# Performance work log

Hardware: AMD Instinct MI355X
Metric: run time of the kernel (lower is better)

The kernel has to match this reference:

```python
import jax, jax.numpy as jnp
import numpy as np

N, E = 50000, 800000
IN_D, HID, H1, OUT_D, H2, EDGE_D = 64, 16, 8, 64, 2, 1
NEG_SLOPE = 0.2


def gatv2_layer(x, src, dst, edge_attr, Wl, Wr, We, att, bias, concat):
    """PyG GATv2Conv (add_self_loops=False, share_weights=False), eval mode (no dropout)."""
    n = x.shape[0]
    H, C = att.shape
    xl = (x @ Wl).reshape(n, H, C)            # source transform
    xr = (x @ Wr).reshape(n, H, C)            # target transform
    ee = (edge_attr @ We).reshape(-1, H, C)   # edge embedding
    z = jax.nn.leaky_relu(xl[src] + xr[dst] + ee, NEG_SLOPE)  # [E,H,C]
    score = jnp.einsum('ehc,hc->eh', z, att)                  # [E,H]
    # softmax over incoming edges per target node
    m = jax.ops.segment_max(score, dst, num_segments=n)
    m = jnp.where(jnp.isfinite(m), m, 0.0)
    a = jnp.exp(score - m[dst])
    denom = jax.ops.segment_sum(a, dst, num_segments=n)
    alpha = a / (denom[dst] + 1e-16)                          # [E,H]
    msg = xl[src] * alpha[..., None]                          # [E,H,C]
    out = jax.ops.segment_sum(msg, dst, num_segments=n)       # [N,H,C]
    if concat:
        return out.reshape(n, H * C) + bias
    return out.mean(axis=1) + bias


def layer_norm(x, g, b):
    mu = x.mean(-1, keepdims=True)
    var = ((x - mu) ** 2).mean(-1, keepdims=True)
    return (x - mu) * jax.lax.rsqrt(var + 1e-5) * g + b


def setup_inputs() -> dict:
    key = jax.random.key(0)
    ks = jax.random.split(key, 24)
    def w(k, *shape):
        fan_in = shape[0]
        return jax.random.normal(k, shape, dtype=jnp.float32) * (1.0 / np.sqrt(fan_in))
    inp = {
        'x': jax.random.normal(ks[0], (N, IN_D), dtype=jnp.float32),
        'edge_index': jax.random.randint(ks[1], (2, E), 0, N, dtype=jnp.int64),
        'edge_attr': jax.random.normal(ks[2], (E, EDGE_D), dtype=jnp.float32),
        # layer 1 (heads=8, out=16, concat)
        'w1_l': w(ks[3], IN_D, H1 * HID), 'w1_r': w(ks[4], IN_D, H1 * HID),
        'w1_e': w(ks[5], EDGE_D, H1 * HID),
        'att1': jax.random.normal(ks[6], (H1, HID), dtype=jnp.float32) * 0.1,
        'b1': jnp.zeros((H1 * HID,), dtype=jnp.float32),
        # layer 2 (heads=2, out=64, mean)
        'w2_l': w(ks[7], H1 * HID, H2 * OUT_D), 'w2_r': w(ks[8], H1 * HID, H2 * OUT_D),
        'w2_e': w(ks[9], EDGE_D, H2 * OUT_D),
        'att2': jax.random.normal(ks[10], (H2, OUT_D), dtype=jnp.float32) * 0.1,
        'b2': jnp.zeros((OUT_D,), dtype=jnp.float32),
        # classifier: Linear + LayerNorm + GELU + ResidualBlockv2
        'wc': w(ks[11], OUT_D, OUT_D), 'bc': jnp.zeros((OUT_D,), dtype=jnp.float32),
        'ln_g': jnp.ones((OUT_D,), dtype=jnp.float32), 'ln_b': jnp.zeros((OUT_D,), dtype=jnp.float32),
        'wr': w(ks[12], OUT_D, OUT_D), 'br': jnp.zeros((OUT_D,), dtype=jnp.float32),
        'lnr_g': jnp.ones((OUT_D,), dtype=jnp.float32), 'lnr_b': jnp.zeros((OUT_D,), dtype=jnp.float32),
    }
    return inp


def reference(x, edge_index, edge_attr, w1_l, w1_r, w1_e, att1, b1,
              w2_l, w2_r, w2_e, att2, b2, wc, bc, ln_g, ln_b, wr, br, lnr_g, lnr_b):
    src, dst = edge_index[0], edge_index[1]
    h = jax.nn.relu(gatv2_layer(x, src, dst, edge_attr, w1_l, w1_r, w1_e, att1, b1, True))
    h = jax.nn.relu(gatv2_layer(h, src, dst, edge_attr, w2_l, w2_r, w2_e, att2, b2, False))
    h = jax.nn.gelu(layer_norm(h @ wc + bc, ln_g, ln_b), approximate=False)
    # ResidualBlockv2: Linear -> LayerNorm -> GELU with residual skip
    h = h + jax.nn.gelu(layer_norm(h @ wr + br, lnr_g, lnr_b), approximate=False)
    return h
```

## Files before the change

### kernel.cpp

```cpp
#include <hip/hip_runtime.h>
#include <math.h>

#define NNODE 50000
#define NEDGE 800000
#define NBLK 196

__device__ __forceinline__ float wsum64(float v) {
    #pragma unroll
    for (int m = 32; m >= 1; m >>= 1) v += __shfl_xor(v, m, 64);
    return v;
}

__device__ __forceinline__ float gelu_exact(float x) {
    return 0.5f * x * (1.0f + erff(x * 0.70710678118654752f));
}

__device__ __forceinline__ float lrelu(float z) { return z > 0.f ? z : 0.2f * z; }

__global__ void fill_u32(unsigned* __restrict__ p, unsigned v, int n) {
    int i = blockIdx.x * blockDim.x + threadIdx.x;
    if (i < n) p[i] = v;
}

__global__ __launch_bounds__(256) void build_deg(const int* __restrict__ ei, int* __restrict__ deg) {
    int e = blockIdx.x * 256 + threadIdx.x;
    if (e >= NEDGE) return;
    atomicAdd(&deg[ei[NEDGE + e]], 1);
}

__global__ __launch_bounds__(256) void scan1(const int* __restrict__ deg,
                                             int* __restrict__ partial,
                                             int* __restrict__ bsum) {
    __shared__ int tmp[256];
    int t = threadIdx.x;
    int gid = blockIdx.x * 256 + t;
    int v = (gid < NNODE) ? deg[gid] : 0;
    tmp[t] = v;
    __syncthreads();
    #pragma unroll
    for (int off = 1; off < 256; off <<= 1) {
        int u = (t >= off) ? tmp[t - off] : 0;
        __syncthreads();
        tmp[t] += u;
        __syncthreads();
    }
    if (gid < NNODE) partial[gid] = tmp[t] - v;
    if (t == 255) bsum[blockIdx.x] = tmp[255];
}

__global__ __launch_bounds__(256) void scan2(int* __restrict__ bsum, int* __restrict__ boff) {
    __shared__ int tmp[256];
    int t = threadIdx.x;
    int v = (t < NBLK) ? bsum[t] : 0;
    tmp[t] = v;
    __syncthreads();
    #pragma unroll
    for (int off = 1; off < 256; off <<= 1) {
        int u = (t >= off) ? tmp[t - off] : 0;
        __syncthreads();
        tmp[t] += u;
        __syncthreads();
    }
    if (t < NBLK) boff[t] = tmp[t] - v;
}

__global__ __launch_bounds__(256) void scan3(const int* __restrict__ partial,
                                             const int* __restrict__ boff,
                                             int* __restrict__ base,
                                             int* __restrict__ cursor) {
    int gid = blockIdx.x * 256 + threadIdx.x;
    if (gid < NNODE) {
        int b = partial[gid] + boff[blockIdx.x];
        base[gid] = b;
        cursor[gid] = b;
    }
    if (gid == 0) base[NNODE] = NEDGE;
}

__global__ __launch_bounds__(256) void scatter_edges(const int* __restrict__ ei,
                                                     const float* __restrict__ ea,
                                                     int* __restrict__ cursor,
                                                     int2* __restrict__ se) {
    int e = blockIdx.x * 256 + threadIdx.x;
    if (e >= NEDGE) return;
    int d = ei[NEDGE + e];
    int i = atomicAdd(&cursor[d], 1);
    se[i] = make_int2(ei[e], __float_as_int(ea[e]));
}

template<int K>
__global__ __launch_bounds__(256) void node_xform(const float* __restrict__ in,
                                                  const float* __restrict__ wl,
                                                  const float* __restrict__ wr,
                                                  float* __restrict__ xl,
                                                  float* __restrict__ xr) {
    __shared__ float xrow[32][K];
    int t = threadIdx.x;
    int n0 = blockIdx.x * 32;
    for (int idx = t; idx < 32 * (K / 4); idx += 256) {
        int row = idx / (K / 4), c4 = idx % (K / 4);
        float4 v = make_float4(0.f, 0.f, 0.f, 0.f);
        if (n0 + row < NNODE) v = ((const float4*)(in + (size_t)(n0 + row) * K))[c4];
        ((float4*)xrow[row])[c4] = v;
    }
    __syncthreads();
    int cg = t & 63, ns = t >> 6;
    const float* wsel = (cg < 32) ? wl : wr;
    float* osel = (cg < 32) ? xl : xr;
    int ccol = (cg & 31) * 4;
    const float* wp = wsel + ccol;
    const float* xbase = xrow[ns * 8];
    float4 acc[8];
    #pragma unroll
    for (int k = 0; k < 8; ++k) acc[k] = make_float4(0.f, 0.f, 0.f, 0.f);
    for (int i = 0; i < K; i += 4) {
        float4 w0 = *(const float4*)(wp + (size_t)(i + 0) * 128);
        float4 w1 = *(const float4*)(wp + (size_t)(i + 1) * 128);
        float4 w2 = *(const float4*)(wp + (size_t)(i + 2) * 128);
        float4 w3 = *(const float4*)(wp + (size_t)(i + 3) * 128);
        #pragma unroll
        for (int k = 0; k < 8; ++k) {
            float4 xv = *(const float4*)(xbase + (size_t)k * K + i);
            acc[k].x += xv.x * w0.x + xv.y * w1.x + xv.z * w2.x + xv.w * w3.x;
            acc[k].y += xv.x * w0.y + xv.y * w1.y + xv.z * w2.y + xv.w * w3.y;
            acc[k].z += xv.x * w0.z + xv.y * w1.z + xv.z * w2.z + xv.w * w3.z;
            acc[k].w += xv.x * w0.w + xv.y * w1.w + xv.z * w2.w + xv.w * w3.w;
        }
    }
    #pragma unroll
    for (int k = 0; k < 8; ++k) {
        int n = n0 + ns * 8 + k;
        if (n < NNODE) *(float4*)(osel + (size_t)n * 128 + ccol) = acc[k];
    }
}

__global__ __launch_bounds__(256) void fused1(const int* __restrict__ base,
                                              const int2* __restrict__ se,
                                              const float* __restrict__ xl,
                                              const float* __restrict__ xr,
                                              const float* __restrict__ w1e,
                                              const float* __restrict__ att1,
                                              const float* __restrict__ b1,
                                              float* __restrict__ h1) {
    int t = threadIdx.x;
    int wv = t >> 6, ln = t & 63;
    int half = ln >> 5, sub = ln & 31;
    int n = blockIdx.x * 4 + wv;
    int ch = sub * 4;
    float4 xrv = *(const float4*)(xr + (size_t)n * 128 + ch);
    float4 wev = *(const float4*)(w1e + ch);
    float4 atv = *(const float4*)(att1 + ch);
    int i0 = base[n], i1 = base[n + 1];
    float m = -1e30f, den = 0.f;
    float4 o = make_float4(0.f, 0.f, 0.f, 0.f);
    int i = i0 + half;
    if (i < i1) {
        int2 r = se[i];
        float4 xv = *(const float4*)(xl + (size_t)r.x * 128 + ch);
        float a = __int_as_float(r.y);
        for (i += 2; i < i1; i += 2) {
            int2 rn = se[i];
            float4 nxv = *(const float4*)(xl + (size_t)rn.x * 128 + ch);
            float na = __int_as_float(rn.y);
            float part = lrelu(fmaf(a, wev.x, xv.x + xrv.x)) * atv.x
                       + lrelu(fmaf(a, wev.y, xv.y + xrv.y)) * atv.y
                       + lrelu(fmaf(a, wev.z, xv.z + xrv.z)) * atv.z
                       + lrelu(fmaf(a, wev.w, xv.w + xrv.w)) * atv.w;
            part += __shfl_xor(part, 1, 64);
            part += __shfl_xor(part, 2, 64);
            float mn = fmaxf(m, part);
            float sc = __expf(m - mn);
            float p  = __expf(part - mn);
            den = den * sc + p;
            o.x = o.x * sc + p * xv.x;
            o.y = o.y * sc + p * xv.y;
            o.z = o.z * sc + p * xv.z;
            o.w = o.w * sc + p * xv.w;
            m = mn;
            xv = nxv; a = na;
        }
        float part = lrelu(fmaf(a, wev.x, xv.x + xrv.x)) * atv.x
                   + lrelu(fmaf(a, wev.y, xv.y + xrv.y)) * atv.y
                   + lrelu(fmaf(a, wev.z, xv.z + xrv.z)) * atv.z
                   + lrelu(fmaf(a, wev.w, xv.w + xrv.w)) * atv.w;
        part += __shfl_xor(part, 1, 64);
        part += __shfl_xor(part, 2, 64);
        float mn = fmaxf(m, part);
        float sc = __expf(m - mn);
        float p  = __expf(part - mn);
        den = den * sc + p;
        o.x = o.x * sc + p * xv.x;
        o.y = o.y * sc + p * xv.y;
        o.z = o.z * sc + p * xv.z;
        o.w = o.w * sc + p * xv.w;
        m = mn;
    }
    float m2   = __shfl_xor(m, 32, 64);
    float den2 = __shfl_xor(den, 32, 64);
    float4 o2;
    o2.x = __shfl_xor(o.x, 32, 64);
    o2.y = __shfl_xor(o.y, 32, 64);
    o2.z = __shfl_xor(o.z, 32, 64);
    o2.w = __shfl_xor(o.w, 32, 64);
    float mn = fmaxf(m, m2);
    float s1 = __expf(m - mn), s2 = __expf(m2 - mn);
    den = den * s1 + den2 * s2;
    float inv = 1.f / (den + 1e-16f);
    if (half == 0) {
        float4 bv = *(const float4*)(b1 + ch);
        float4 res;
        res.x = fmaxf((o.x * s1 + o2.x * s2) * inv + bv.x, 0.f);
        res.y = fmaxf((o.y * s1 + o2.y * s2) * inv + bv.y, 0.f);
        res.z = fmaxf((o.z * s1 + o2.z * s2) * inv + bv.z, 0.f);
        res.w = fmaxf((o.w * s1 + o2.w * s2) * inv + bv.w, 0.f);
        *(float4*)(h1 + (size_t)n * 128 + ch) = res;
    }
}

__global__ __launch_bounds__(256) void fused2(const int* __restrict__ base,
                                              const int2* __restrict__ se,
                                              const float* __restrict__ xl,
                                              const float* __restrict__ xr,
                                              const float* __restrict__ w2e,
                                              const float* __restrict__ att2,
                                              const float* __restrict__ b2,
                                              float* __restrict__ h2) {
    int t = threadIdx.x;
    int wv = t >> 6, ln = t & 63;
    int half = ln >> 5, sub = ln & 31;
    int n = blockIdx.x * 4 + wv;
    int ch = sub * 4;
    float4 xrv = *(const float4*)(xr + (size_t)n * 128 + ch);
    float4 wev = *(const float4*)(w2e + ch);
    float4 atv = *(const float4*)(att2 + ch);
    int i0 = base[n], i1 = base[n + 1];
    float m = -1e30f, den = 0.f;
    float4 o = make_float4(0.f, 0.f, 0.f, 0.f);
    int i = i0 + half;
    if (i < i1) {
        int2 r = se[i];
        float4 xv = *(const float4*)(xl + (size_t)r.x * 128 + ch);
        float a = __int_as_float(r.y);
        for (i += 2; i < i1; i += 2) {
            int2 rn = se[i];
            float4 nxv = *(const float4*)(xl + (size_t)rn.x * 128 + ch);
            float na = __int_as_float(rn.y);
            float part = lrelu(fmaf(a, wev.x, xv.x + xrv.x)) * atv.x
                       + lrelu(fmaf(a, wev.y, xv.y + xrv.y)) * atv.y
                       + lrelu(fmaf(a, wev.z, xv.z + xrv.z)) * atv.z
                       + lrelu(fmaf(a, wev.w, xv.w + xrv.w)) * atv.w;
            part += __shfl_xor(part, 1, 64);
            part += __shfl_xor(part, 2, 64);
            part += __shfl_xor(part, 4, 64);
            part += __shfl_xor(part, 8, 64);
            float mn = fmaxf(m, part);
            float sc = __expf(m - mn);
            float p  = __expf(part - mn);
            den = den * sc + p;
            o.x = o.x * sc + p * xv.x;
            o.y = o.y * sc + p * xv.y;
            o.z = o.z * sc + p * xv.z;
            o.w = o.w * sc + p * xv.w;
            m = mn;
            xv = nxv; a = na;
        }
        float part = lrelu(fmaf(a, wev.x, xv.x + xrv.x)) * atv.x
                   + lrelu(fmaf(a, wev.y, xv.y + xrv.y)) * atv.y
                   + lrelu(fmaf(a, wev.z, xv.z + xrv.z)) * atv.z
                   + lrelu(fmaf(a, wev.w, xv.w + xrv.w)) * atv.w;
        part += __shfl_xor(part, 1, 64);
        part += __shfl_xor(part, 2, 64);
        part += __shfl_xor(part, 4, 64);
        part += __shfl_xor(part, 8, 64);
        float mn = fmaxf(m, part);
        float sc = __expf(m - mn);
        float p  = __expf(part - mn);
        den = den * sc + p;
        o.x = o.x * sc + p * xv.x;
        o.y = o.y * sc + p * xv.y;
        o.z = o.z * sc + p * xv.z;
        o.w = o.w * sc + p * xv.w;
        m = mn;
    }
    float m2   = __shfl_xor(m, 32, 64);
    float den2 = __shfl_xor(den, 32, 64);
    float4 o2;
    o2.x = __shfl_xor(o.x, 32, 64);
    o2.y = __shfl_xor(o.y, 32, 64);
    o2.z = __shfl_xor(o.z, 32, 64);
    o2.w = __shfl_xor(o.w, 32, 64);
    float mn = fmaxf(m, m2);
    float s1 = __expf(m - mn), s2 = __expf(m2 - mn);
    den = den * s1 + den2 * s2;
    float inv = 1.f / (den + 1e-16f);
    float4 v;
    v.x = (o.x * s1 + o2.x * s2) * inv;
    v.y = (o.y * s1 + o2.y * s2) * inv;
    v.z = (o.z * s1 + o2.z * s2) * inv;
    v.w = (o.w * s1 + o2.w * s2) * inv;
    float4 u;
    u.x = __shfl_xor(v.x, 16, 64);
    u.y = __shfl_xor(v.y, 16, 64);
    u.z = __shfl_xor(v.z, 16, 64);
    u.w = __shfl_xor(v.w, 16, 64);
    if (half == 0 && sub < 16) {
        float4 bv = *(const float4*)(b2 + ch);
        float4 res;
        res.x = fmaxf(0.5f * (v.x + u.x) + bv.x, 0.f);
        res.y = fmaxf(0.5f * (v.y + u.y) + bv.y, 0.f);
        res.z = fmaxf(0.5f * (v.z + u.z) + bv.z, 0.f);
        res.w = fmaxf(0.5f * (v.w + u.w) + bv.w, 0.f);
        *(float4*)(h2 + (size_t)n * 64 + ch) = res;
    }
}

__global__ __launch_bounds__(256) void classifier(const float* __restrict__ h2,
                                                  const float* __restrict__ wc,
                                                  const float* __restrict__ bc,
                                                  const float* __restrict__ lng,
                                                  const float* __restrict__ lnb,
                                                  const float* __restrict__ wrr,
                                                  const float* __restrict__ brr,
                                                  const float* __restrict__ lrg,
                                                  const float* __restrict__ lrb,
                                                  float* __restrict__ out) {
    __shared__ float swc[4096];
    __shared__ float swr[4096];
    __shared__ float svec[384];
    __shared__ float rowA[4][64];
    __shared__ float rowB[4][64];
    int t = threadIdx.x;
    for (int i = t; i < 4096; i += 256) { swc[i] = wc[i]; swr[i] = wrr[i]; }
    if (t < 64) {
        svec[t]       = bc[t];
        svec[64 + t]  = lng[t];
        svec[128 + t] = lnb[t];
        svec[192 + t] = brr[t];
        svec[256 + t] = lrg[t];
        svec[320 + t] = lrb[t];
    }
    __syncthreads();
    int wv = t >> 6, ln = t & 63;
    #pragma unroll
    for (int k = 0; k < 4; ++k) {
        int n = blockIdx.x * 16 + wv * 4 + k;
        rowA[wv][ln] = h2[(size_t)n * 64 + ln];
        float acc = svec[ln];
        #pragma unroll 4
        for (int j = 0; j < 64; j += 4) {
            float4 hv = *(const float4*)&rowA[wv][j];
            acc += hv.x * swc[(j + 0) * 64 + ln] + hv.y * swc[(j + 1) * 64 + ln]
                 + hv.z * swc[(j + 2) * 64 + ln] + hv.w * swc[(j + 3) * 64 + ln];
        }
        float mu = wsum64(acc) * (1.f / 64.f);
        float dv = acc - mu;
        float var = wsum64(dv * dv) * (1.f / 64.f);
        float y = dv * rsqrtf(var + 1e-5f) * svec[64 + ln] + svec[128 + ln];
        float g1 = gelu_exact(y);
        rowB[wv][ln] = g1;
        float acc2 = svec[192 + ln];
        #pragma unroll 4
        for (int j = 0; j < 64; j += 4) {
            float4 hv = *(const float4*)&rowB[wv][j];
            acc2 += hv.x * swr[(j + 0) * 64 + ln] + hv.y * swr[(j + 1) * 64 + ln]
                  + hv.z * swr[(j + 2) * 64 + ln] + hv.w * swr[(j + 3) * 64 + ln];
        }
        float mu2 = wsum64(acc2) * (1.f / 64.f);
        float dv2 = acc2 - mu2;
        float var2 = wsum64(dv2 * dv2) * (1.f / 64.f);
        float y2 = dv2 * rsqrtf(var2 + 1e-5f) * svec[256 + ln] + svec[320 + ln];
        float g2 = gelu_exact(y2);
        out[(size_t)n * 64 + ln] = g1 + g2;
    }
}

extern "C" void kernel_launch(void* const* d_in, const int* in_sizes, int n_in,
                              void* d_out, int out_size, void* d_ws, size_t ws_size,
                              hipStream_t stream) {
    const float* x    = (const float*)d_in[0];
    const int*   ei   = (const int*)d_in[1];
    const float* ea   = (const float*)d_in[2];
    const float* w1l  = (const float*)d_in[3];
    const float* w1r  = (const float*)d_in[4];
    const float* w1e  = (const float*)d_in[5];
    const float* att1 = (const float*)d_in[6];
    const float* b1   = (const float*)d_in[7];
    const float* w2l  = (const float*)d_in[8];
    const float* w2r  = (const float*)d_in[9];
    const float* w2e  = (const float*)d_in[10];
    const float* att2 = (const float*)d_in[11];
    const float* b2   = (const float*)d_in[12];
    const float* wc   = (const float*)d_in[13];
    const float* bc   = (const float*)d_in[14];
    const float* lng  = (const float*)d_in[15];
    const float* lnb  = (const float*)d_in[16];
    const float* wr   = (const float*)d_in[17];
    const float* br   = (const float*)d_in[18];
    const float* lrg  = (const float*)d_in[19];
    const float* lrb  = (const float*)d_in[20];

    float* ws = (float*)d_ws;
    const size_t N128 = (size_t)NNODE * 128;
    float* xl = ws;
    float* xr = xl + N128;
    float* h1 = xr + N128;
    float* h2 = h1 + N128;
    int2*  se      = (int2*)(h2 + (size_t)NNODE * 64);
    int*   deg     = (int*)(se + NEDGE);
    int*   partial = deg + NNODE;
    int*   base    = partial + NNODE;
    int*   cursor  = base + NNODE + 1;
    int*   bsum    = cursor + NNODE;
    int*   boff    = bsum + 256;

    const int EB  = NEDGE / 256;
    const int NBX = (NNODE + 31) / 32;
    const int NB4 = NNODE / 4;

    fill_u32<<<NBLK, 256, 0, stream>>>((unsigned*)deg, 0u, NNODE);
    build_deg<<<EB, 256, 0, stream>>>(ei, deg);
    scan1<<<NBLK, 256, 0, stream>>>(deg, partial, bsum);
    scan2<<<1, 256, 0, stream>>>(bsum, boff);
    scan3<<<NBLK, 256, 0, stream>>>(partial, boff, base, cursor);
    scatter_edges<<<EB, 256, 0, stream>>>(ei, ea, cursor, se);

    node_xform<64><<<NBX, 256, 0, stream>>>(x, w1l, w1r, xl, xr);
    fused1<<<NB4, 256, 0, stream>>>(base, se, xl, xr, w1e, att1, b1, h1);

    node_xform<128><<<NBX, 256, 0, stream>>>(h1, w2l, w2r, xl, xr);
    fused2<<<NB4, 256, 0, stream>>>(base, se, xl, xr, w2e, att2, b2, h2);

    classifier<<<NNODE / 16, 256, 0, stream>>>(h2, wc, bc, lng, lnb, wr, br, lrg, lrb,
                                               (float*)d_out);
}
```

Before: 352.6 us.

## Restructure classifier as 64-node register-tiled GEMM with weights read from global

The classifier now processes 64 nodes per block instead of 16 and computes both 64x64 linear layers as a register-tiled GEMM. Each thread produces a 4x4 output tile from float4 weight loads taken straight from global/L1, instead of first staging both 16 KB weight matrices into LDS for every block. LayerNorm and GELU run as a separate per-row warp pass over shared memory. This removes the per-block weight staging and raises arithmetic reuse, at the cost of extra barriers, fewer blocks, and weight reads that depend on cache hits.

```diff
diff --git a/kernel.cpp b/kernel.cpp
--- a/kernel.cpp
+++ b/kernel.cpp
@@ -324,53 +324,86 @@
                                                   const float* __restrict__ lrg,
                                                   const float* __restrict__ lrb,
                                                   float* __restrict__ out) {
-    __shared__ float swc[4096];
-    __shared__ float swr[4096];
-    __shared__ float svec[384];
-    __shared__ float rowA[4][64];
-    __shared__ float rowB[4][64];
-    int t = threadIdx.x;
-    for (int i = t; i < 4096; i += 256) { swc[i] = wc[i]; swr[i] = wrr[i]; }
-    if (t < 64) {
-        svec[t]       = bc[t];
-        svec[64 + t]  = lng[t];
-        svec[128 + t] = lnb[t];
-        svec[192 + t] = brr[t];
-        svec[256 + t] = lrg[t];
-        svec[320 + t] = lrb[t];
-    }
-    __syncthreads();
+    __shared__ float hA[64][68];
+    __shared__ float hB[64][68];
+    int t = threadIdx.x;
+    int n0 = blockIdx.x * 64;
+    for (int idx = t; idx < 64 * 16; idx += 256) {
+        int row = idx >> 4, c4 = idx & 15;
+        float4 v = make_float4(0.f, 0.f, 0.f, 0.f);
+        if (n0 + row < NNODE) v = ((const float4*)(h2 + (size_t)(n0 + row) * 64))[c4];
+        *(float4*)(&hA[row][c4 * 4]) = v;
+    }
+    __syncthreads();
+    int cg = t & 15, ng = t >> 4;
+    int ccol = cg * 4;
     int wv = t >> 6, ln = t & 63;
-    #pragma unroll
-    for (int k = 0; k < 4; ++k) {
-        int n = blockIdx.x * 16 + wv * 4 + k;
-        rowA[wv][ln] = h2[(size_t)n * 64 + ln];
-        float acc = svec[ln];
-        #pragma unroll 4
-        for (int j = 0; j < 64; j += 4) {
-            float4 hv = *(const float4*)&rowA[wv][j];
-            acc += hv.x * swc[(j + 0) * 64 + ln] + hv.y * swc[(j + 1) * 64 + ln]
-                 + hv.z * swc[(j + 2) * 64 + ln] + hv.w * swc[(j + 3) * 64 + ln];
+    float lngv = lng[ln], lnbv = lnb[ln], lrgv = lrg[ln], lrbv = lrb[ln];
+    {
+        float4 bv = *(const float4*)(bc + ccol);
+        float4 acc[4];
+        #pragma unroll
+        for (int k = 0; k < 4; ++k) acc[k] = bv;
+        for (int i = 0; i < 64; i += 4) {
+            float4 w0 = *(const float4*)(wc + (size_t)(i + 0) * 64 + ccol);
+            float4 w1 = *(const float4*)(wc + (size_t)(i + 1) * 64 + ccol);
+            float4 w2 = *(const float4*)(wc + (size_t)(i + 2) * 64 + ccol);
+            float4 w3 = *(const float4*)(wc + (size_t)(i + 3) * 64 + ccol);
+            #pragma unroll
+            for (int k = 0; k < 4; ++k) {
+                float4 hv = *(const float4*)(&hA[ng * 4 + k][i]);
+                acc[k].x += hv.x * w0.x + hv.y * w1.x + hv.z * w2.x + hv.w * w3.x;
+                acc[k].y += hv.x * w0.y + hv.y * w1.y + hv.z * w2.y + hv.w * w3.y;
+                acc[k].z += hv.x * w0.z + hv.y * w1.z + hv.z * w2.z + hv.w * w3.z;
+                acc[k].w += hv.x * w0.w + hv.y * w1.w + hv.z * w2.w + hv.w * w3.w;
+            }
         }
-        float mu = wsum64(acc) * (1.f / 64.f);
-        float dv = acc - mu;
+        #pragma unroll
+        for (int k = 0; k < 4; ++k) *(float4*)(&hB[ng * 4 + k][ccol]) = acc[k];
+    }
+    __syncthreads();
+    for (int k = 0; k < 16; ++k) {
+        int n = wv * 16 + k;
+        float v = hB[n][ln];
+        float mu = wsum64(v) * (1.f / 64.f);
+        float dv = v - mu;
         float var = wsum64(dv * dv) * (1.f / 64.f);
-        float y = dv * rsqrtf(var + 1e-5f) * svec[64 + ln] + svec[128 + ln];
-        float g1 = gelu_exact(y);
-        rowB[wv][ln] = g1;
-        float acc2 = svec[192 + ln];
-        #pragma unroll 4
-        for (int j = 0; j < 64; j += 4) {
-            float4 hv = *(const float4*)&rowB[wv][j];
-            acc2 += hv.x * swr[(j + 0) * 64 + ln] + hv.y * swr[(j + 1) * 64 + ln]
-                  + hv.z * swr[(j + 2) * 64 + ln] + hv.w * swr[(j + 3) * 64 + ln];
+        float y = dv * rsqrtf(var + 1e-5f) * lngv + lnbv;
+        hA[n][ln] = gelu_exact(y);
+    }
+    __syncthreads();
+    {
+        float4 bv = *(const float4*)(brr + ccol);
+        float4 acc[4];
+        #pragma unroll
+        for (int k = 0; k < 4; ++k) acc[k] = bv;
+        for (int i = 0; i < 64; i += 4) {
+            float4 w0 = *(const float4*)(wrr + (size_t)(i + 0) * 64 + ccol);
+            float4 w1 = *(const float4*)(wrr + (size_t)(i + 1) * 64 + ccol);
+            float4 w2 = *(const float4*)(wrr + (size_t)(i + 2) * 64 + ccol);
+            float4 w3 = *(const float4*)(wrr + (size_t)(i + 3) * 64 + ccol);
+            #pragma unroll
+            for (int k = 0; k < 4; ++k) {
+                float4 hv = *(const float4*)(&hA[ng * 4 + k][i]);
+                acc[k].x += hv.x * w0.x + hv.y * w1.x + hv.z * w2.x + hv.w * w3.x;
+                acc[k].y += hv.x * w0.y + hv.y * w1.y + hv.z * w2.y + hv.w * w3.y;
+                acc[k].z += hv.x * w0.z + hv.y * w1.z + hv.z * w2.z + hv.w * w3.z;
+                acc[k].w += hv.x * w0.w + hv.y * w1.w + hv.z * w2.w + hv.w * w3.w;
+            }
         }
-        float mu2 = wsum64(acc2) * (1.f / 64.f);
-        float dv2 = acc2 - mu2;
-        float var2 = wsum64(dv2 * dv2) * (1.f / 64.f);
-        float y2 = dv2 * rsqrtf(var2 + 1e-5f) * svec[256 + ln] + svec[320 + ln];
-        float g2 = gelu_exact(y2);
-        out[(size_t)n * 64 + ln] = g1 + g2;
+        #pragma unroll
+        for (int k = 0; k < 4; ++k) *(float4*)(&hB[ng * 4 + k][ccol]) = acc[k];
+    }
+    __syncthreads();
+    for (int k = 0; k < 16; ++k) {
+        int n = wv * 16 + k;
+        float v = hB[n][ln];
+        float mu = wsum64(v) * (1.f / 64.f);
+        float dv = v - mu;
+        float var = wsum64(dv * dv) * (1.f / 64.f);
+        float y = dv * rsqrtf(var + 1e-5f) * lrgv + lrbv;
+        float g2 = gelu_exact(y);
+        if (n0 + n < NNODE) out[(size_t)(n0 + n) * 64 + ln] = hA[n][ln] + g2;
     }
 }
 
@@ -416,6 +449,7 @@
     const int EB  = NEDGE / 256;
     const int NBX = (NNODE + 31) / 32;
     const int NB4 = NNODE / 4;
+    const int NBC = (NNODE + 63) / 64;
 
     fill_u32<<<NBLK, 256, 0, stream>>>((unsigned*)deg, 0u, NNODE);
     build_deg<<<EB, 256, 0, stream>>>(ei, deg);
@@ -430,6 +464,6 @@
     node_xform<128><<<NBX, 256, 0, stream>>>(h1, w2l, w2r, xl, xr);
     fused2<<<NB4, 256, 0, stream>>>(base, se, xl, xr, w2e, att2, b2, h2);
 
-    classifier<<<NNODE / 16, 256, 0, stream>>>(h2, wc, bc, lng, lnb, wr, br, lrg, lrb,
-                                               (float*)d_out);
-}
+    classifier<<<NBC, 256, 0, stream>>>(h2, wc, bc, lng, lnb, wr, br, lrg, lrb,
+                                        (float*)d_out);
+}
```

After: 401.6 us. 1.14x slower.

## Keep classifier weights in registers and broadcast rows via readlane

Applied to the files above, without the earlier changes.

The classifier kernel now holds each lane's column of both 64x64 weight matrices in registers and broadcasts row elements with readlane, so it no longer stages the weights and rows in shared memory. It runs a persistent grid of 640 blocks, and each wave loops over nodes with a grid stride. This removes the per-block reload of 32KB of weights into LDS across 3125 blocks and the LDS traffic in the inner loop. In exchange it uses about 128+ VGPRs per thread, which lowers occupancy and may cause spills.

```diff
diff --git a/kernel.cpp b/kernel.cpp
--- a/kernel.cpp
+++ b/kernel.cpp
@@ -16,6 +16,10 @@
 }
 
 __device__ __forceinline__ float lrelu(float z) { return z > 0.f ? z : 0.2f * z; }
+
+__device__ __forceinline__ float bcast(float v, int lane) {
+    return __uint_as_float(__builtin_amdgcn_readlane(__float_as_uint(v), lane));
+}
 
 __global__ void fill_u32(unsigned* __restrict__ p, unsigned v, int n) {
     int i = blockIdx.x * blockDim.x + threadIdx.x;
@@ -314,62 +318,55 @@
     }
 }
 
-__global__ __launch_bounds__(256) void classifier(const float* __restrict__ h2,
-                                                  const float* __restrict__ wc,
-                                                  const float* __restrict__ bc,
-                                                  const float* __restrict__ lng,
-                                                  const float* __restrict__ lnb,
-                                                  const float* __restrict__ wrr,
-                                                  const float* __restrict__ brr,
-                                                  const float* __restrict__ lrg,
-                                                  const float* __restrict__ lrb,
-                                                  float* __restrict__ out) {
-    __shared__ float swc[4096];
-    __shared__ float swr[4096];
-    __shared__ float svec[384];
-    __shared__ float rowA[4][64];
-    __shared__ float rowB[4][64];
-    int t = threadIdx.x;
-    for (int i = t; i < 4096; i += 256) { swc[i] = wc[i]; swr[i] = wrr[i]; }
-    if (t < 64) {
-        svec[t]       = bc[t];
-        svec[64 + t]  = lng[t];
-        svec[128 + t] = lnb[t];
-        svec[192 + t] = brr[t];
-        svec[256 + t] = lrg[t];
-        svec[320 + t] = lrb[t];
-    }
-    __syncthreads();
-    int wv = t >> 6, ln = t & 63;
-    #pragma unroll
-    for (int k = 0; k < 4; ++k) {
-        int n = blockIdx.x * 16 + wv * 4 + k;
-        rowA[wv][ln] = h2[(size_t)n * 64 + ln];
-        float acc = svec[ln];
-        #pragma unroll 4
+__global__ __launch_bounds__(256) void classifier_reg(const float* __restrict__ h2,
+                                                      const float* __restrict__ wc,
+                                                      const float* __restrict__ bc,
+                                                      const float* __restrict__ lng,
+                                                      const float* __restrict__ lnb,
+                                                      const float* __restrict__ wrr,
+                                                      const float* __restrict__ brr,
+                                                      const float* __restrict__ lrg,
+                                                      const float* __restrict__ lrb,
+                                                      float* __restrict__ out,
+                                                      int nwaves_total) {
+    int t = threadIdx.x;
+    int ln = t & 63;
+    int wid = (blockIdx.x * 256 + t) >> 6;
+    float wcr[64], wrg[64];
+    #pragma unroll
+    for (int j = 0; j < 64; ++j) wcr[j] = wc[(size_t)j * 64 + ln];
+    #pragma unroll
+    for (int j = 0; j < 64; ++j) wrg[j] = wrr[(size_t)j * 64 + ln];
+    float bcv = bc[ln], lngv = lng[ln], lnbv = lnb[ln];
+    float brv = brr[ln], lrgv = lrg[ln], lrbv = lrb[ln];
+    for (int n = wid; n < NNODE; n += nwaves_total) {
+        float h = h2[(size_t)n * 64 + ln];
+        float a0 = bcv, a1 = 0.f, a2 = 0.f, a3 = 0.f;
+        #pragma unroll
         for (int j = 0; j < 64; j += 4) {
-            float4 hv = *(const float4*)&rowA[wv][j];
-            acc += hv.x * swc[(j + 0) * 64 + ln] + hv.y * swc[(j + 1) * 64 + ln]
-                 + hv.z * swc[(j + 2) * 64 + ln] + hv.w * swc[(j + 3) * 64 + ln];
+            a0 = fmaf(bcast(h, j + 0), wcr[j + 0], a0);
+            a1 = fmaf(bcast(h, j + 1), wcr[j + 1], a1);
+            a2 = fmaf(bcast(h, j + 2), wcr[j + 2], a2);
+            a3 = fmaf(bcast(h, j + 3), wcr[j + 3], a3);
         }
+        float acc = (a0 + a1) + (a2 + a3);
         float mu = wsum64(acc) * (1.f / 64.f);
         float dv = acc - mu;
         float var = wsum64(dv * dv) * (1.f / 64.f);
-        float y = dv * rsqrtf(var + 1e-5f) * svec[64 + ln] + svec[128 + ln];
-        float g1 = gelu_exact(y);
-        rowB[wv][ln] = g1;
-        float acc2 = svec[192 + ln];
-        #pragma unroll 4
+        float g1 = gelu_exact(dv * rsqrtf(var + 1e-5f) * lngv + lnbv);
+        float b0 = brv, b1v = 0.f, b2v = 0.f, b3v = 0.f;
+        #pragma unroll
         for (int j = 0; j < 64; j += 4) {
-            float4 hv = *(const float4*)&rowB[wv][j];
-            acc2 += hv.x * swr[(j + 0) * 64 + ln] + hv.y * swr[(j + 1) * 64 + ln]
-                  + hv.z * swr[(j + 2) * 64 + ln] + hv.w * swr[(j + 3) * 64 + ln];
+            b0  = fmaf(bcast(g1, j + 0), wrg[j + 0], b0);
+            b1v = fmaf(bcast(g1, j + 1), wrg[j + 1], b1v);
+            b2v = fmaf(bcast(g1, j + 2), wrg[j + 2], b2v);
+            b3v = fmaf(bcast(g1, j + 3), wrg[j + 3], b3v);
         }
+        float acc2 = (b0 + b1v) + (b2v + b3v);
         float mu2 = wsum64(acc2) * (1.f / 64.f);
         float dv2 = acc2 - mu2;
         float var2 = wsum64(dv2 * dv2) * (1.f / 64.f);
-        float y2 = dv2 * rsqrtf(var2 + 1e-5f) * svec[256 + ln] + svec[320 + ln];
-        float g2 = gelu_exact(y2);
+        float g2 = gelu_exact(dv2 * rsqrtf(var2 + 1e-5f) * lrgv + lrbv);
         out[(size_t)n * 64 + ln] = g1 + g2;
     }
 }
@@ -416,6 +413,7 @@
     const int EB  = NEDGE / 256;
     const int NBX = (NNODE + 31) / 32;
     const int NB4 = NNODE / 4;
+    const int CBLK = 640;
 
     fill_u32<<<NBLK, 256, 0, stream>>>((unsigned*)deg, 0u, NNODE);
     build_deg<<<EB, 256, 0, stream>>>(ei, deg);
@@ -430,6 +428,6 @@
     node_xform<128><<<NBX, 256, 0, stream>>>(h1, w2l, w2r, xl, xr);
     fused2<<<NB4, 256, 0, stream>>>(base, se, xl, xr, w2e, att2, b2, h2);
 
-    classifier<<<NNODE / 16, 256, 0, stream>>>(h2, wc, bc, lng, lnb, wr, br, lrg, lrb,
-                                               (float*)d_out);
-}
+    classifier_reg<<<CBLK, 256, 0, stream>>>(h2, wc, bc, lng, lnb, wr, br, lrg, lrb,
+                                             (float*)d_out, CBLK * 4);
+}
```

New measurement: 344.9 us. 2.2% less time.
